# Performance work log

Measured on AMD Instinct MI355X. Metric: run time of the kernel, lower is better.

## Reference

```python
import jax, jax.numpy as jnp
import numpy as np

B, S, E, H = 2, 2048, 1024, 16
D = E // H  # 64 head dim


def _rope_tables(seq_len, d_head, base=10000.0):
    half = d_head // 2
    inv_freq = 1.0 / (base ** (np.arange(0, half, dtype=np.float32) / half))
    t = np.arange(seq_len, dtype=np.float32)
    ang = np.outer(t, inv_freq)  # [S, d_head/2]
    return jnp.asarray(np.cos(ang)), jnp.asarray(np.sin(ang))


def setup_inputs() -> dict:
    key = jax.random.key(0)
    k1, k2, k3 = jax.random.split(key, 3)
    x = jax.random.normal(k1, (B, S, E), dtype=jnp.float32)
    w_qkv = jax.random.normal(k2, (E, 3 * E), dtype=jnp.float32) / np.sqrt(E)
    w_out = jax.random.normal(k3, (E, E), dtype=jnp.float32) / np.sqrt(E)
    freqs_cos, freqs_sin = _rope_tables(S, D)
    return {"x": x, "w_qkv": w_qkv, "w_out": w_out,
            "freqs_cos": freqs_cos, "freqs_sin": freqs_sin}


def _apply_rope(x, cos, sin):
    # x: [B, H, S, D]; cos/sin: [S, D/2] -> broadcast [1, 1, S, D/2]
    xr = x.reshape(*x.shape[:-1], D // 2, 2)
    x0, x1 = xr[..., 0], xr[..., 1]
    c = cos[None, None, :, :]
    s = sin[None, None, :, :]
    out = jnp.stack([x0 * c - x1 * s, x0 * s + x1 * c], axis=-1)
    return out.reshape(x.shape)


def reference(x, w_qkv, w_out, freqs_cos, freqs_sin):
    qkv = x @ w_qkv  # [B, S, 3E]
    q, k, v = jnp.split(qkv, 3, axis=-1)
    def heads(t):
        return t.reshape(B, S, H, D).transpose(0, 2, 1, 3)  # [B, H, S, D]
    q, k, v = heads(q), heads(k), heads(v)
    q = _apply_rope(q, freqs_cos, freqs_sin)
    k = _apply_rope(k, freqs_cos, freqs_sin)
    scale = 1.0 / np.sqrt(D).astype(np.float32)
    scores = jnp.einsum('bhsd,bhtd->bhst', q, k) * scale  # [B, H, S, S]
    causal = jnp.tril(jnp.ones((S, S), dtype=bool))
    scores = jnp.where(causal[None, None], scores, jnp.finfo(scores.dtype).min)
    attn = jax.nn.softmax(scores, axis=-1)
    out = jnp.einsum('bhst,bhtd->bhsd', attn, v)  # [B, H, S, D]
    out = out.transpose(0, 2, 1, 3).reshape(B, S, E)
    return out @ w_out  # dropout is identity in eval mode
```

## Files before the change

kernel.cpp:

```cpp
#include <hip/hip_runtime.h>
#include <cstdint>
#include <cstddef>

typedef unsigned short u16;
typedef __attribute__((ext_vector_type(8))) short bf16x8;
typedef __attribute__((ext_vector_type(8))) unsigned short u16x8;
typedef __attribute__((ext_vector_type(4))) float f32x4;

static constexpr int Bc = 2, Sc = 2048, Ec = 1024, Hc = 16, Dc = 64;

__device__ __forceinline__ float bf2f(u16 v) {
    unsigned u = ((unsigned)v) << 16;
    float f; __builtin_memcpy(&f, &u, 4); return f;
}
__device__ __forceinline__ u16 f2bf(float f) {
    unsigned u; __builtin_memcpy(&u, &f, 4);
    u += 0x7fffu + ((u >> 16) & 1u);
    return (u16)(u >> 16);
}
__device__ __forceinline__ bf16x8 as_bf(u16x8 v) { return __builtin_bit_cast(bf16x8, v); }

__global__ void cast_f32_bf16(const float* __restrict__ in, u16* __restrict__ out, int n) {
    int i = (blockIdx.x * blockDim.x + threadIdx.x) * 4;
    if (i < n) {
        float4 v = *reinterpret_cast<const float4*>(in + i);
        ushort4 o;
        o.x = f2bf(v.x); o.y = f2bf(v.y); o.z = f2bf(v.z); o.w = f2bf(v.w);
        *reinterpret_cast<ushort4*>(out + i) = o;
    }
}

__global__ void transpose_cast(const float* __restrict__ in, u16* __restrict__ out,
                               int R, int C) {
    __shared__ float tile[32][33];
    int tx = threadIdx.x, ty = threadIdx.y;
    int c0 = blockIdx.x * 32, r0 = blockIdx.y * 32;
    tile[ty][tx] = in[(size_t)(r0 + ty) * C + c0 + tx];
    __syncthreads();
    out[(size_t)(c0 + ty) * R + r0 + tx] = f2bf(tile[tx][ty]);
}

template <int OUT_BF16>
__global__ __launch_bounds__(256) void gemm_bt(const u16* __restrict__ A,
                                               const u16* __restrict__ Bt,
                                               void* __restrict__ Cout,
                                               int M, int N, int K) {
    constexpr int BK = 32;
    __shared__ u16 As[128][BK];
    __shared__ u16 Bs[128][BK];
    const int m0 = blockIdx.x * 128, n0 = blockIdx.y * 128;
    const int t = threadIdx.x;
    const int lane = t & 63, w = t >> 6;
    const int wr = w >> 1, wc = w & 1;
    const int l15 = lane & 15, lhi = lane >> 4;
    const int lrow = lane >> 2, lcol = (lane & 3) * 8;

    f32x4 acc[4][4] = {};

    for (int k0 = 0; k0 < K; k0 += BK) {
#pragma unroll
        for (int i = 0; i < 2; i++) {
            const u16* ap = A + (size_t)(m0 + w * 32 + i * 16 + lrow) * K + k0 + lcol;
            __builtin_amdgcn_global_load_lds(
                (const __attribute__((address_space(1))) unsigned int*)ap,
                (__attribute__((address_space(3))) unsigned int*)&As[w * 32 + i * 16][0],
                16, 0, 0);
            const u16* bp = Bt + (size_t)(n0 + w * 32 + i * 16 + lrow) * K + k0 + lcol;
            __builtin_amdgcn_global_load_lds(
                (const __attribute__((address_space(1))) unsigned int*)bp,
                (__attribute__((address_space(3))) unsigned int*)&Bs[w * 32 + i * 16][0],
                16, 0, 0);
        }
        __syncthreads();

        bf16x8 af[4], bfv[4];
#pragma unroll
        for (int i = 0; i < 4; i++)
            af[i] = as_bf(*reinterpret_cast<const u16x8*>(&As[wr * 64 + i * 16 + l15][lhi * 8]));
#pragma unroll
        for (int j = 0; j < 4; j++)
            bfv[j] = as_bf(*reinterpret_cast<const u16x8*>(&Bs[wc * 64 + j * 16 + l15][lhi * 8]));
#pragma unroll
        for (int i = 0; i < 4; i++)
#pragma unroll
            for (int j = 0; j < 4; j++)
                acc[i][j] = __builtin_amdgcn_mfma_f32_16x16x32_bf16(af[i], bfv[j], acc[i][j], 0, 0, 0);
        __syncthreads();
    }

#pragma unroll
    for (int i = 0; i < 4; i++)
#pragma unroll
        for (int j = 0; j < 4; j++)
#pragma unroll
            for (int r = 0; r < 4; r++) {
                int row = m0 + wr * 64 + i * 16 + lhi * 4 + r;
                int col = n0 + wc * 64 + j * 16 + l15;
                float v = acc[i][j][r];
                if (OUT_BF16)
                    ((u16*)Cout)[(size_t)row * N + col] = f2bf(v);
                else
                    ((float*)Cout)[(size_t)row * N + col] = v;
            }
}

__global__ void rope_pack(const u16* __restrict__ qkv,
                          const float* __restrict__ fcos, const float* __restrict__ fsin,
                          u16* __restrict__ Qb, u16* __restrict__ Kb) {
    int g = blockIdx.x * blockDim.x + threadIdx.x;
    int dg = g & 3;
    int h = (g >> 2) & 15;
    int row = g >> 6;
    int b = row >> 11, s = row & 2047;
    const float QS = 0.18033688011f;

    const u16* qp = qkv + (size_t)row * 3072 + h * 64 + dg * 16;
    u16x8 q0 = *reinterpret_cast<const u16x8*>(qp);
    u16x8 q1 = *reinterpret_cast<const u16x8*>(qp + 8);
    u16x8 k0 = *reinterpret_cast<const u16x8*>(qp + 1024);
    u16x8 k1 = *reinterpret_cast<const u16x8*>(qp + 1032);

    const float* cp = fcos + (size_t)s * 32 + dg * 8;
    const float* sp = fsin + (size_t)s * 32 + dg * 8;
    float cs[8], sn[8];
#pragma unroll
    for (int p = 0; p < 8; p++) { cs[p] = cp[p]; sn[p] = sp[p]; }

    u16 qi[16], ki[16], qo[16], ko[16];
#pragma unroll
    for (int j = 0; j < 8; j++) { qi[j] = q0[j]; qi[j + 8] = q1[j]; ki[j] = k0[j]; ki[j + 8] = k1[j]; }
#pragma unroll
    for (int p = 0; p < 8; p++) {
        float x0 = bf2f(qi[2 * p]), x1 = bf2f(qi[2 * p + 1]);
        qo[2 * p]     = f2bf((x0 * cs[p] - x1 * sn[p]) * QS);
        qo[2 * p + 1] = f2bf((x0 * sn[p] + x1 * cs[p]) * QS);
        float y0 = bf2f(ki[2 * p]), y1 = bf2f(ki[2 * p + 1]);
        ko[2 * p]     = f2bf(y0 * cs[p] - y1 * sn[p]);
        ko[2 * p + 1] = f2bf(y0 * sn[p] + y1 * cs[p]);
    }

    size_t dst = ((size_t)(b * 16 + h) * 2048 + s) * 64 + dg * 16;
    u16x8 qa, qb2, ka, kb2;
#pragma unroll
    for (int j = 0; j < 8; j++) { qa[j] = qo[j]; qb2[j] = qo[j + 8]; ka[j] = ko[j]; kb2[j] = ko[j + 8]; }
    *reinterpret_cast<u16x8*>(Qb + dst) = qa;
    *reinterpret_cast<u16x8*>(Qb + dst + 8) = qb2;
    *reinterpret_cast<u16x8*>(Kb + dst) = ka;
    *reinterpret_cast<u16x8*>(Kb + dst + 8) = kb2;
}

__global__ __launch_bounds__(256) void vtrans(const u16* __restrict__ qkv,
                                              u16* __restrict__ VT) {
    __shared__ u16 tile[64][70];
    const int bh = blockIdx.y, b = bh >> 4, h = bh & 15;
    const int s0 = blockIdx.x * 64;
    const int t = threadIdx.x;
    const int si = t >> 2, dc = (t & 3) * 16;
    const u16* src = qkv + (size_t)(b * 2048 + s0 + si) * 3072 + 2048 + h * 64 + dc;
    *reinterpret_cast<u16x8*>(&tile[si][dc])     = *reinterpret_cast<const u16x8*>(src);
    *reinterpret_cast<u16x8*>(&tile[si][dc + 8]) = *reinterpret_cast<const u16x8*>(src + 8);
    __syncthreads();
    const int d = t >> 2, sc = (t & 3) * 16;
    u16x8 v0, v1;
#pragma unroll
    for (int j = 0; j < 8; j++) { v0[j] = tile[sc + j][d]; v1[j] = tile[sc + 8 + j][d]; }
    size_t dst = ((size_t)bh * 64 + d) * 2048 + s0 + sc;
    *reinterpret_cast<u16x8*>(VT + dst)     = v0;
    *reinterpret_cast<u16x8*>(VT + dst + 8) = v1;
}


__device__ __forceinline__ void load_ktile(const u16* __restrict__ Kp, int t0,
                                           int l15, int lhi, bf16x8 (&kd)[8]) {
#pragma unroll
    for (int cb = 0; cb < 4; cb++) {
        const u16* kp = Kp + (size_t)(t0 + cb * 16 + l15) * 64 + lhi * 8;
        kd[cb * 2 + 0] = as_bf(*reinterpret_cast<const u16x8*>(kp));
        kd[cb * 2 + 1] = as_bf(*reinterpret_cast<const u16x8*>(kp + 32));
    }
}

__device__ __forceinline__ void attn_tile(int t0, int nt0, bool diag, int q0,
                                          const u16* __restrict__ Kp,
                                          const u16* __restrict__ Vp,
                                          int l15, int lhi,
                                          const bf16x8 (&kc_)[8], bf16x8 (&kn_)[8],
                                          const bf16x8 (&qf)[2][2], bf16x8 onesf,
                                          f32x4 (&o)[2][4], f32x4 (&os)[2],
                                          u16* __restrict__ PsW) {
    load_ktile(Kp, nt0, l15, lhi, kn_);

    f32x4 s[2][4];
#pragma unroll
    for (int qa = 0; qa < 2; qa++)
#pragma unroll
        for (int cb = 0; cb < 4; cb++) {
            f32x4 v = {-14.0f, -14.0f, -14.0f, -14.0f};
            v = __builtin_amdgcn_mfma_f32_16x16x32_bf16(qf[qa][0], kc_[cb * 2 + 0], v, 0, 0, 0);
            v = __builtin_amdgcn_mfma_f32_16x16x32_bf16(qf[qa][1], kc_[cb * 2 + 1], v, 0, 0, 0);
            s[qa][cb] = v;
        }

    bf16x8 vf[8];
#pragma unroll
    for (int db = 0; db < 4; db++)
#pragma unroll
        for (int kc2 = 0; kc2 < 2; kc2++)
            vf[db * 2 + kc2] = as_bf(*reinterpret_cast<const u16x8*>(
                Vp + (size_t)(db * 16 + l15) * 2048 + t0 + kc2 * 32 + lhi * 8));

    if (diag) {
#pragma unroll
        for (int qa = 0; qa < 2; qa++)
#pragma unroll
            for (int cb = 0; cb < 4; cb++) {
                const int tg = t0 + cb * 16 + l15;
#pragma unroll
                for (int r = 0; r < 4; r++) {
                    const int qg = q0 + qa * 16 + lhi * 4 + r;
                    if (tg > qg) s[qa][cb][r] = -1e30f;
                }
            }
    }

#pragma unroll
    for (int qa = 0; qa < 2; qa++)
#pragma unroll
        for (int cb = 0; cb < 4; cb++)
#pragma unroll
            for (int r = 0; r < 4; r++) {
                float p = __builtin_amdgcn_exp2f(s[qa][cb][r]);
                unsigned pb; __builtin_memcpy(&pb, &p, 4);
                PsW[(qa * 16 + lhi * 4 + r) * 70 + cb * 16 + l15] = (u16)(pb >> 16);
            }
    asm volatile("s_waitcnt lgkmcnt(0)" ::: "memory");
    __builtin_amdgcn_sched_barrier(0);

#pragma unroll
    for (int qa = 0; qa < 2; qa++) {
        bf16x8 pf0 = as_bf(*reinterpret_cast<const u16x8*>(&PsW[(qa * 16 + l15) * 70 + lhi * 8]));
        bf16x8 pf1 = as_bf(*reinterpret_cast<const u16x8*>(&PsW[(qa * 16 + l15) * 70 + 32 + lhi * 8]));
        os[qa] = __builtin_amdgcn_mfma_f32_16x16x32_bf16(pf0, onesf, os[qa], 0, 0, 0);
        os[qa] = __builtin_amdgcn_mfma_f32_16x16x32_bf16(pf1, onesf, os[qa], 0, 0, 0);
#pragma unroll
        for (int db = 0; db < 4; db++) {
            o[qa][db] = __builtin_amdgcn_mfma_f32_16x16x32_bf16(pf0, vf[db * 2 + 0], o[qa][db], 0, 0, 0);
            o[qa][db] = __builtin_amdgcn_mfma_f32_16x16x32_bf16(pf1, vf[db * 2 + 1], o[qa][db], 0, 0, 0);
        }
    }
}

__global__ __launch_bounds__(64, 1) void attn_fwd3(const u16* __restrict__ Qb,
                                                   const u16* __restrict__ Kb,
                                                   const u16* __restrict__ VTb,
                                                   u16* __restrict__ attn_out) {
    __shared__ u16 Ps[32 * 70];
    const int lane = threadIdx.x & 63;
    const int l15 = lane & 15, lhi = lane >> 4;
    const int id = blockIdx.x;
    const int bh = (id & 7) + 8 * ((id >> 3) & 3);
    const int pair = id >> 5;
    const int b = bh >> 4, h = bh & 15;
    const u16* Kp = Kb + (size_t)bh * (Sc * Dc);
    const u16* Vp = VTb + (size_t)bh * (Sc * Dc);

    u16x8 onesu;
#pragma unroll
    for (int j = 0; j < 8; j++) onesu[j] = 0x3F80;
    const bf16x8 onesf = as_bf(onesu);

#pragma unroll
    for (int pass = 0; pass < 2; pass++) {
        const int qc = pass == 0 ? 63 - pair : pair;
        const int q0 = qc * 32;

        bf16x8 qf[2][2];
#pragma unroll
        for (int qa = 0; qa < 2; qa++)
#pragma unroll
            for (int kc = 0; kc < 2; kc++)
                qf[qa][kc] = as_bf(*reinterpret_cast<const u16x8*>(
                    Qb + (size_t)bh * (Sc * Dc) + (size_t)(q0 + qa * 16 + l15) * 64 + kc * 32 + lhi * 8));

        f32x4 o[2][4] = {};
        f32x4 os[2] = {};

        const int ntiles = qc / 2 + 1;
        const int last = (ntiles - 1) * 64;

        bf16x8 ka[8], kb2[8];
        load_ktile(Kp, 0, l15, lhi, ka);

        int kt = 0;
        while (true) {
            int t0 = kt * 64;
            int nt0 = (t0 < last) ? t0 + 64 : last;
            attn_tile(t0, nt0, t0 == last, q0, Kp, Vp, l15, lhi, ka, kb2, qf, onesf, o, os, Ps);
            if (++kt >= ntiles) break;
            t0 = kt * 64;
            nt0 = (t0 < last) ? t0 + 64 : last;
            attn_tile(t0, nt0, t0 == last, q0, Kp, Vp, l15, lhi, kb2, ka, qf, onesf, o, os, Ps);
            if (++kt >= ntiles) break;
        }

#pragma unroll
        for (int qa = 0; qa < 2; qa++)
#pragma unroll
            for (int r = 0; r < 4; r++) {
                const int qg = q0 + qa * 16 + lhi * 4 + r;
                const float inv = 1.0f / os[qa][r];
                const size_t orow = ((size_t)(b * 2048 + qg)) * 1024 + h * 64;
#pragma unroll
                for (int db = 0; db < 4; db++)
                    attn_out[orow + db * 16 + l15] = f2bf(o[qa][db][r] * inv);
            }
    }
}

extern "C" void kernel_launch(void* const* d_in, const int* in_sizes, int n_in,
                              void* d_out, int out_size, void* d_ws, size_t ws_size,
                              hipStream_t stream) {
    const float* x     = (const float*)d_in[0];
    const float* w_qkv = (const float*)d_in[1];
    const float* w_out = (const float*)d_in[2];
    const float* fcos  = (const float*)d_in[3];
    const float* fsin  = (const float*)d_in[4];
    float* out = (float*)d_out;

    char* ws = (char*)d_ws;
    u16* xb    = (u16*)(ws);
    u16* wqkvT = (u16*)(ws + 8388608);
    u16* woutT = (u16*)(ws + 14680064);
    u16* qkvb  = (u16*)(ws + 16777216);
    u16* Qb    = (u16*)(ws + 41943040);
    u16* Kb    = (u16*)(ws + 50331648);
    u16* VTb   = (u16*)(ws + 58720256);
    u16* attnb = (u16*)(ws + 67108864);

    cast_f32_bf16<<<4096, 256, 0, stream>>>(x, xb, Bc * Sc * Ec);
    transpose_cast<<<dim3(96, 32), dim3(32, 32), 0, stream>>>(w_qkv, wqkvT, 1024, 3072);
    transpose_cast<<<dim3(32, 32), dim3(32, 32), 0, stream>>>(w_out, woutT, 1024, 1024);
    gemm_bt<1><<<dim3(32, 24), 256, 0, stream>>>(xb, wqkvT, qkvb, 4096, 3072, 1024);
    rope_pack<<<1024, 256, 0, stream>>>(qkvb, fcos, fsin, Qb, Kb);
    vtrans<<<dim3(32, 32), 256, 0, stream>>>(qkvb, VTb);
    attn_fwd3<<<1024, 64, 0, stream>>>(Qb, Kb, VTb, attnb);
    gemm_bt<0><<<dim3(32, 8), 256, 0, stream>>>(attnb, woutT, out, 4096, 1024, 1024);
}
```

Baseline: 226.9 us.

## Split each attention block's KV tiles across four waves with LDS reduction

The attention kernel moves from one wave per block handling a pair of query chunks sequentially to four waves that split the combined 33 KV tiles of both chunks (9/8/8/8). Partial O and row sums are accumulated into shared memory with atomicAdd, then normalized and written out with vectorized stores. The aim is more parallelism per block and shorter serial dependency chains per wave. The cost is LDS atomics and extra synchronization. The fixed max offset (-14) means partial sums can be added directly without rescaling.

```diff
diff --git a/kernel.cpp b/kernel.cpp
--- a/kernel.cpp
+++ b/kernel.cpp
@@ -169,9 +169,8 @@
     *reinterpret_cast<u16x8*>(VT + dst + 8) = v1;
 }
 
-
-__device__ __forceinline__ void load_ktile(const u16* __restrict__ Kp, int t0,
-                                           int l15, int lhi, bf16x8 (&kd)[8]) {
+__device__ __forceinline__ void load_ktile7(const u16* __restrict__ Kp, int t0,
+                                            int l15, int lhi, bf16x8 (&kd)[8]) {
 #pragma unroll
     for (int cb = 0; cb < 4; cb++) {
         const u16* kp = Kp + (size_t)(t0 + cb * 16 + l15) * 64 + lhi * 8;
@@ -180,15 +179,15 @@
     }
 }
 
-__device__ __forceinline__ void attn_tile(int t0, int nt0, bool diag, int q0,
-                                          const u16* __restrict__ Kp,
-                                          const u16* __restrict__ Vp,
-                                          int l15, int lhi,
-                                          const bf16x8 (&kc_)[8], bf16x8 (&kn_)[8],
-                                          const bf16x8 (&qf)[2][2], bf16x8 onesf,
-                                          f32x4 (&o)[2][4], f32x4 (&os)[2],
-                                          u16* __restrict__ PsW) {
-    load_ktile(Kp, nt0, l15, lhi, kn_);
+__device__ __forceinline__ void attn_tile7(int t0, int nt0, bool diag, int q0,
+                                           const u16* __restrict__ Kp,
+                                           const u16* __restrict__ Vp,
+                                           int l15, int lhi,
+                                           const bf16x8 (&kc_)[8], bf16x8 (&kn_)[8],
+                                           const bf16x8 (&qf)[2][2], bf16x8 onesf,
+                                           f32x4 (&o)[2][4], f32x4 (&os)[2],
+                                           u16* __restrict__ PsW) {
+    load_ktile7(Kp, nt0, l15, lhi, kn_);
 
     f32x4 s[2][4];
 #pragma unroll
@@ -250,29 +249,47 @@
     }
 }
 
-__global__ __launch_bounds__(64, 1) void attn_fwd3(const u16* __restrict__ Qb,
-                                                   const u16* __restrict__ Kb,
-                                                   const u16* __restrict__ VTb,
-                                                   u16* __restrict__ attn_out) {
-    __shared__ u16 Ps[32 * 70];
-    const int lane = threadIdx.x & 63;
+__global__ __launch_bounds__(256) void attn_fwd7(const u16* __restrict__ Qb,
+                                                 const u16* __restrict__ Kb,
+                                                 const u16* __restrict__ VTb,
+                                                 u16* __restrict__ attn_out) {
+    __shared__ u16 Ps[4][32 * 70];
+    __shared__ float Om[2][32][64];
+    __shared__ float Ol[2][32];
+
+    const int t = threadIdx.x, lane = t & 63, w = t >> 6;
     const int l15 = lane & 15, lhi = lane >> 4;
+
     const int id = blockIdx.x;
     const int bh = (id & 7) + 8 * ((id >> 3) & 3);
-    const int pair = id >> 5;
+    const int p = id >> 5;
     const int b = bh >> 4, h = bh & 15;
+    const u16* Qp = Qb + (size_t)bh * (Sc * Dc);
     const u16* Kp = Kb + (size_t)bh * (Sc * Dc);
     const u16* Vp = VTb + (size_t)bh * (Sc * Dc);
+    u16* PsW = &Ps[w][0];
+
+    for (int i = t; i < 2 * 32 * 64; i += 256) ((float*)Om)[i] = 0.f;
+    if (t < 64) ((float*)Ol)[t] = 0.f;
+    __syncthreads();
 
     u16x8 onesu;
 #pragma unroll
     for (int j = 0; j < 8; j++) onesu[j] = 0x3F80;
     const bf16x8 onesf = as_bf(onesu);
 
-#pragma unroll
-    for (int pass = 0; pass < 2; pass++) {
-        const int qc = pass == 0 ? 63 - pair : pair;
+    const int nh = ((63 - p) >> 1) + 1;
+    const int g0 = w ? 9 + (w - 1) * 8 : 0;
+    const int g1 = w ? g0 + 8 : 9;
+
+    for (int seg = 0; seg < 2; seg++) {
+        const int a0 = seg ? (g0 > nh ? g0 : nh) : g0;
+        const int a1 = seg ? g1 : (g1 < nh ? g1 : nh);
+        if (a0 >= a1) continue;
+        const int qc = seg ? p : 63 - p;
         const int q0 = qc * 32;
+        const int ktoff = seg ? nh : 0;
+        const int ntl = seg ? 33 - nh : nh;
 
         bf16x8 qf[2][2];
 #pragma unroll
@@ -280,40 +297,65 @@
 #pragma unroll
             for (int kc = 0; kc < 2; kc++)
                 qf[qa][kc] = as_bf(*reinterpret_cast<const u16x8*>(
-                    Qb + (size_t)bh * (Sc * Dc) + (size_t)(q0 + qa * 16 + l15) * 64 + kc * 32 + lhi * 8));
+                    Qp + (size_t)(q0 + qa * 16 + l15) * 64 + kc * 32 + lhi * 8));
 
         f32x4 o[2][4] = {};
         f32x4 os[2] = {};
 
-        const int ntiles = qc / 2 + 1;
-        const int last = (ntiles - 1) * 64;
-
         bf16x8 ka[8], kb2[8];
-        load_ktile(Kp, 0, l15, lhi, ka);
-
-        int kt = 0;
+        const int lastkt = ntl - 1;
+        load_ktile7(Kp, (a0 - ktoff) * 64, l15, lhi, ka);
+
+        int g = a0;
         while (true) {
+            int kt = g - ktoff;
             int t0 = kt * 64;
-            int nt0 = (t0 < last) ? t0 + 64 : last;
-            attn_tile(t0, nt0, t0 == last, q0, Kp, Vp, l15, lhi, ka, kb2, qf, onesf, o, os, Ps);
-            if (++kt >= ntiles) break;
+            int nt0 = (kt < lastkt && g + 1 < a1) ? t0 + 64 : t0;
+            attn_tile7(t0, nt0, kt == lastkt, q0, Kp, Vp, l15, lhi, ka, kb2, qf, onesf, o, os, PsW);
+            if (++g >= a1) break;
+            kt = g - ktoff;
             t0 = kt * 64;
-            nt0 = (t0 < last) ? t0 + 64 : last;
-            attn_tile(t0, nt0, t0 == last, q0, Kp, Vp, l15, lhi, kb2, ka, qf, onesf, o, os, Ps);
-            if (++kt >= ntiles) break;
-        }
-
+            nt0 = (kt < lastkt && g + 1 < a1) ? t0 + 64 : t0;
+            attn_tile7(t0, nt0, kt == lastkt, q0, Kp, Vp, l15, lhi, kb2, ka, qf, onesf, o, os, PsW);
+            if (++g >= a1) break;
+        }
+
+        const int ci = seg;
 #pragma unroll
         for (int qa = 0; qa < 2; qa++)
 #pragma unroll
             for (int r = 0; r < 4; r++) {
-                const int qg = q0 + qa * 16 + lhi * 4 + r;
-                const float inv = 1.0f / os[qa][r];
-                const size_t orow = ((size_t)(b * 2048 + qg)) * 1024 + h * 64;
+                const int row = qa * 16 + lhi * 4 + r;
+                if (l15 == 0) atomicAdd(&Ol[ci][row], os[qa][r]);
 #pragma unroll
                 for (int db = 0; db < 4; db++)
-                    attn_out[orow + db * 16 + l15] = f2bf(o[qa][db][r] * inv);
+                    atomicAdd(&Om[ci][row][db * 16 + l15], o[qa][db][r]);
             }
+    }
+
+    __syncthreads();
+
+    {
+        const int c = w >> 1, sub = w & 1;
+        const int row = sub * 16 + (lane >> 2);
+        const int colq = (lane & 3) * 16;
+        const int qg = (c ? p : 63 - p) * 32 + row;
+        const float inv = 1.0f / Ol[c][row];
+        f32x4 v0 = *reinterpret_cast<const f32x4*>(&Om[c][row][colq]);
+        f32x4 v1 = *reinterpret_cast<const f32x4*>(&Om[c][row][colq + 4]);
+        f32x4 v2 = *reinterpret_cast<const f32x4*>(&Om[c][row][colq + 8]);
+        f32x4 v3 = *reinterpret_cast<const f32x4*>(&Om[c][row][colq + 12]);
+        u16x8 o0, o1;
+#pragma unroll
+        for (int j = 0; j < 4; j++) {
+            o0[j]     = f2bf(v0[j] * inv);
+            o0[j + 4] = f2bf(v1[j] * inv);
+            o1[j]     = f2bf(v2[j] * inv);
+            o1[j + 4] = f2bf(v3[j] * inv);
+        }
+        const size_t obase = ((size_t)(b * 2048 + qg)) * 1024 + h * 64 + colq;
+        *reinterpret_cast<u16x8*>(attn_out + obase)     = o0;
+        *reinterpret_cast<u16x8*>(attn_out + obase + 8) = o1;
     }
 }
 
@@ -343,6 +385,6 @@
     gemm_bt<1><<<dim3(32, 24), 256, 0, stream>>>(xb, wqkvT, qkvb, 4096, 3072, 1024);
     rope_pack<<<1024, 256, 0, stream>>>(qkvb, fcos, fsin, Qb, Kb);
     vtrans<<<dim3(32, 32), 256, 0, stream>>>(qkvb, VTb);
-    attn_fwd3<<<1024, 64, 0, stream>>>(Qb, Kb, VTb, attnb);
+    attn_fwd7<<<1024, 256, 0, stream>>>(Qb, Kb, VTb, attnb);
     gemm_bt<0><<<dim3(32, 8), 256, 0, stream>>>(attnb, woutT, out, 4096, 1024, 1024);
 }
```

Result: slower. 277.6 us (+22.3%).
